# Performance work log

Measured on AMD Instinct MI355X. Metric: run time of the kernel, lower is better.

## Reference

```python
import jax, jax.numpy as jnp
import numpy as np

N, E, D, H, O = 50000, 800000, 128, 256, 64
BN_EPS = 1e-5


def setup_inputs() -> dict:
    key = jax.random.key(0)
    ks = jax.random.split(key, 12)
    x_indices = jnp.arange(N, dtype=jnp.int64) if jax.config.jax_enable_x64 else jnp.arange(N, dtype=jnp.int32)
    ei = jax.random.randint(ks[0], (2, E), 0, N, dtype=jnp.int32)
    s = lambda k, shape, fan: jax.random.normal(k, shape, dtype=jnp.float32) * (1.0 / np.sqrt(fan))
    return {
        "x_indices": x_indices,
        "ei": ei,
        "emb": jax.random.normal(ks[1], (N, D), dtype=jnp.float32),
        "W1": s(ks[2], (D, H), D), "b1": jnp.zeros((H,), jnp.float32),
        "g1": jnp.ones((H,), jnp.float32), "be1": jnp.zeros((H,), jnp.float32),
        "W2": s(ks[3], (H, H), H), "b2": jnp.zeros((H,), jnp.float32),
        "g2": jnp.ones((H,), jnp.float32), "be2": jnp.zeros((H,), jnp.float32),
        "W3": s(ks[4], (H, O), H), "b3": jnp.zeros((O,), jnp.float32),
    }


def reference(x_indices, ei, emb, W1, b1, g1, be1, W2, b2, g2, be2, W3, b3):
    n = emb.shape[0]
    # GCN normalization with self-loops (PyG GCNConv default):
    loop = jnp.arange(n, dtype=ei.dtype)
    row = jnp.concatenate([ei[0], loop])  # source
    col = jnp.concatenate([ei[1], loop])  # target (aggregation index)
    deg = jax.ops.segment_sum(jnp.ones_like(col, dtype=emb.dtype), col, num_segments=n)
    dinv = jnp.where(deg > 0, 1.0 / jnp.sqrt(jnp.maximum(deg, 1.0)), 0.0)
    norm = dinv[row] * dinv[col]  # [E+N]

    def conv(x, W, b):
        xl = x @ W                                   # [N, d_out]
        msg = xl[row] * norm[:, None]                # gather + scale
        return jax.ops.segment_sum(msg, col, num_segments=n) + b  # scatter-add

    def bn(x, g, be):  # batch-stat BatchNorm1d (training-mode stats)
        m = jnp.mean(x, axis=0)
        v = jnp.var(x, axis=0)
        return (x - m) * (g / jnp.sqrt(v + BN_EPS)) + be

    x = emb[x_indices]
    x = jax.nn.relu(bn(conv(x, W1, b1), g1, be1))
    x = jax.nn.relu(bn(conv(x, W2, b2), g2, be2))
    return conv(x, W3, b3)
```

## Files before the change

kernel.cpp:

```cpp
#include <hip/hip_runtime.h>
#include <hip/hip_bf16.h>

#define Dk 128
#define Hk 256
#define Ok 64
#define BN_EPS 1e-5f
#define NSLICE 64

typedef __attribute__((ext_vector_type(8))) short short8;
typedef __attribute__((ext_vector_type(4))) float f32x4;

static __device__ __forceinline__ float bf2f(ushort u) {
    union { uint32_t i; float f; } c; c.i = ((uint32_t)u) << 16; return c.f;
}
static __device__ __forceinline__ ushort f2bf(float f) {
    union { float f; uint32_t u; } c; c.f = f;
    return (ushort)((c.u + 0x7fffu + ((c.u >> 16) & 1u)) >> 16);
}


#define W1SZ (Dk * Hk)
#define W2SZ (Hk * Hk)
#define W3SZ (Hk * Ok)
#define WBLK ((W1SZ + W2SZ + W3SZ) / 256)
#define STATSP_FLOATS (2 * NSLICE * 512)

__global__ void count_cvt_kernel(const int* __restrict__ ecol, int* __restrict__ cnt, int E,
                                 const float* __restrict__ emb, const int* __restrict__ xidx,
                                 ushort* __restrict__ embb,
                                 const float* __restrict__ W1, const float* __restrict__ W2,
                                 const float* __restrict__ W3, ushort* __restrict__ W1t,
                                 ushort* __restrict__ W2t, ushort* __restrict__ W3t,
                                 float* __restrict__ statsP, int n) {
    const int cntBlocks = (E + 255) >> 8;
    const int embBlocks = (n * (Dk / 8) + 255) >> 8;
    int bid = blockIdx.x;
    if (bid < cntBlocks) {
        int e = bid * 256 + threadIdx.x;
        if (e < E) atomicAdd(&cnt[ecol[e]], 1);
        return;
    }
    bid -= cntBlocks;
    if (bid < embBlocks) {
        int gid = bid * 256 + threadIdx.x;
        int total = n * (Dk / 8);
        if (gid >= total) return;
        int node = gid >> 4, seg = gid & 15;
        int src = xidx[node];
        const float* p = &emb[(size_t)src * Dk + seg * 8];
        float4 lo = *(const float4*)p, hi = *(const float4*)(p + 4);
        ushort r[8] = {f2bf(lo.x), f2bf(lo.y), f2bf(lo.z), f2bf(lo.w),
                       f2bf(hi.x), f2bf(hi.y), f2bf(hi.z), f2bf(hi.w)};
        *(short8*)&embb[(size_t)gid * 8] = *(short8*)r;
        return;
    }
    bid -= embBlocks;
    if (bid < WBLK) {
        int gid = bid * 256 + threadIdx.x;
        if (gid < W1SZ) {
            int c = gid / Dk, k = gid - c * Dk;
            W1t[gid] = f2bf(W1[(size_t)k * Hk + c]);
        } else if (gid < W1SZ + W2SZ) {
            int idx = gid - W1SZ;
            int c = idx / Hk, k = idx - c * Hk;
            W2t[idx] = f2bf(W2[(size_t)k * Hk + c]);
        } else {
            int idx = gid - W1SZ - W2SZ;
            int c = idx / Hk, k = idx - c * Hk;
            W3t[idx] = f2bf(W3[(size_t)k * Ok + c]);
        }
        return;
    }
    bid -= WBLK;
    int idx = bid * 1024 + threadIdx.x * 4;
    if (idx < STATSP_FLOATS)
        *(float4*)&statsP[idx] = make_float4(0.f, 0.f, 0.f, 0.f);
}

__global__ void dinv_bsum_kernel(const int* __restrict__ cnt, float* __restrict__ dinv,
                                 int* __restrict__ fillc, int* __restrict__ bsum, int n) {
    __shared__ int sm[256];
    int i = blockIdx.x * 256 + threadIdx.x;
    int c = (i < n) ? cnt[i] : 0;
    if (i < n) { dinv[i] = rsqrtf((float)c + 1.0f); fillc[i] = 0; }
    sm[threadIdx.x] = c;
    __syncthreads();
    for (int s = 128; s; s >>= 1) {
        if (threadIdx.x < s) sm[threadIdx.x] += sm[threadIdx.x + s];
        __syncthreads();
    }
    if (!threadIdx.x) bsum[blockIdx.x] = sm[0];
}

__global__ void scan_off_kernel(const int* __restrict__ cnt, const int* __restrict__ bsum,
                                int* __restrict__ offv, int n) {
    __shared__ int sm[256];
    __shared__ int sbase;
    int t = threadIdx.x, bidx = blockIdx.x;
    int part = 0;
    for (int j = t; j < bidx; j += 256) part += bsum[j];
    sm[t] = part;
    __syncthreads();
    for (int s = 128; s; s >>= 1) {
        if (t < s) sm[t] += sm[t + s];
        __syncthreads();
    }
    if (t == 0) sbase = sm[0];
    __syncthreads();
    int base = sbase;
    __syncthreads();
    int i = bidx * 256 + t;
    int v = (i < n) ? cnt[i] : 0;
    sm[t] = v;
    __syncthreads();
    for (int s = 1; s < 256; s <<= 1) {
        int add = (t >= s) ? sm[t - s] : 0;
        __syncthreads();
        sm[t] += add;
        __syncthreads();
    }
    if (i < n) offv[i + 1] = base + sm[t];
    if (i == 0) offv[0] = 0;
}

__global__ void fill_kernel(const int* __restrict__ row, const int* __restrict__ col,
                            const int* __restrict__ off, int* __restrict__ fillc,
                            const float* __restrict__ dinv, int2* __restrict__ ep, int E) {
    int e = blockIdx.x * blockDim.x + threadIdx.x;
    if (e < E) {
        int c = col[e], r = row[e];
        int p = atomicAdd(&fillc[c], 1);
        ep[off[c] + p] = make_int2(r, __float_as_int(dinv[r]));
    }
}

__global__ void bn_finalize_kernel(const float* __restrict__ statsP, const float* __restrict__ g,
                                   const float* __restrict__ be, float* __restrict__ ss,
                                   float invn) {
    int f = threadIdx.x;
    float sum = 0.f, sq = 0.f;
    for (int s = 0; s < NSLICE; ++s) {
        sum += statsP[s * 512 + f];
        sq  += statsP[s * 512 + 256 + f];
    }
    float mean = sum * invn;
    float var = sq * invn - mean * mean;
    float sc = g[f] * rsqrtf(var + BN_EPS);
    ss[f] = sc;
    ss[256 + f] = fmaf(-mean, sc, be[f]);
}


template<int KD, int BNT, bool STATS, bool BIAS, bool BN_A>
__global__ __launch_bounds__(256) void gemm128(
    const ushort* __restrict__ A, const ushort* __restrict__ Wt,
    ushort* __restrict__ Cout, int n, int Hout,
    const float* __restrict__ bias, float* __restrict__ statsP,
    const float* __restrict__ ss)
{
    constexpr int WN = (BNT == 128) ? 2 : 1;
    constexpr int MR = (BNT == 128) ? 4 : 2;
    constexpr int NR = 4;
    constexpr int TILE = (128 + BNT) * 32;
    constexpr int NT = KD / 32;
    __shared__ ushort lds[2 * TILE];
    __shared__ float ssc[BN_A ? KD : 1];
    __shared__ float ssh[BN_A ? KD : 1];

    const int tid = threadIdx.x;
    const int lane = tid & 63, wid = tid >> 6;
    const int wr = wid / WN, wc = wid % WN;
    const int lr = lane & 15, lg = lane >> 4;
    const int bm = blockIdx.x * 128;
    const int bn = blockIdx.y * BNT;

    if (BN_A) {
        for (int f = tid; f < KD; f += 256) {
            ssc[f] = ss[f];
            ssh[f] = ss[KD + f];
        }
        __syncthreads();
    }

    auto stage = [&](int buf, int k0) {
        ushort* As = lds + buf * TILE;
        ushort* Bs = As + 128 * 32;
        #pragma unroll
        for (int c = 0; c < 2; ++c) {
            int boff = wid * 2048 + c * 1024 + lane * 16;
            int row = boff >> 6;
            int k8 = (boff >> 4) & 3;
            int grow = bm + row; if (grow >= n) grow = n - 1;
            const ushort* src = &A[(size_t)grow * KD + k0 + k8 * 8];
            if (BN_A) {
                short8 av = *(const short8*)src;
                ushort r[8];
                #pragma unroll
                for (int j = 0; j < 8; ++j) {
                    int kf = k0 + k8 * 8 + j;
                    float v = bf2f((ushort)av[j]);
                    r[j] = f2bf(fmaxf(fmaf(v, ssc[kf], ssh[kf]), 0.f));
                }
                *(short8*)&As[row * 32 + k8 * 8] = *(short8*)r;
            } else {
                __builtin_amdgcn_global_load_lds(
                    (const __attribute__((address_space(1))) void*)src,
                    (__attribute__((address_space(3))) void*)&As[(wid * 2048 + c * 1024) >> 1],
                    16, 0, 0);
            }
        }
        constexpr int BC = BNT * 64 / 4096;
        #pragma unroll
        for (int c = 0; c < BC; ++c) {
            int boff = wid * (BNT * 16) + c * 1024 + lane * 16;
            int col = boff >> 6;
            int k8 = (boff >> 4) & 3;
            const ushort* src = &Wt[(size_t)(bn + col) * KD + k0 + k8 * 8];
            __builtin_amdgcn_global_load_lds(
                (const __attribute__((address_space(1))) void*)src,
                (__attribute__((address_space(3))) void*)&Bs[(wid * (BNT * 16) + c * 1024) >> 1],
                16, 0, 0);
        }
    };

    f32x4 acc[MR][NR] = {};

    stage(0, 0);
    __syncthreads();
    int cur = 0;
    for (int t = 0; t < NT; ++t) {
        if (t + 1 < NT) stage(cur ^ 1, (t + 1) * 32);
        ushort* As = lds + cur * TILE;
        ushort* Bs = As + 128 * 32;
        short8 af[MR], bfr[NR];
        #pragma unroll
        for (int m = 0; m < MR; ++m)
            af[m] = *(const short8*)&As[(wr * MR * 16 + m * 16 + lr) * 32 + lg * 8];
        #pragma unroll
        for (int nn = 0; nn < NR; ++nn)
            bfr[nn] = *(const short8*)&Bs[(wc * NR * 16 + nn * 16 + lr) * 32 + lg * 8];
        #pragma unroll
        for (int m = 0; m < MR; ++m)
            #pragma unroll
            for (int nn = 0; nn < NR; ++nn)
                acc[m][nn] = __builtin_amdgcn_mfma_f32_16x16x32_bf16(af[m], bfr[nn], acc[m][nn], 0, 0, 0);
        __syncthreads();
        cur ^= 1;
    }

    float s[NR], q[NR];
    #pragma unroll
    for (int nn = 0; nn < NR; ++nn) { s[nn] = 0.f; q[nn] = 0.f; }
    #pragma unroll
    for (int nn = 0; nn < NR; ++nn) {
        int col = bn + wc * NR * 16 + nn * 16 + lr;
        float bv = BIAS ? bias[col] : 0.f;
        #pragma unroll
        for (int m = 0; m < MR; ++m) {
            #pragma unroll
            for (int i = 0; i < 4; ++i) {
                int row = bm + wr * MR * 16 + m * 16 + lg * 4 + i;
                if (row < n) {
                    float v = acc[m][nn][i] + bv;
                    Cout[(size_t)row * Hout + col] = f2bf(v);
                    if (STATS) { s[nn] += v; q[nn] += v * v; }
                }
            }
        }
    }
    if (STATS) {
        float* sp = statsP + (size_t)(blockIdx.x & (NSLICE - 1)) * 512;
        #pragma unroll
        for (int nn = 0; nn < NR; ++nn) {
            s[nn] += __shfl_xor(s[nn], 16);
            q[nn] += __shfl_xor(q[nn], 16);
            s[nn] += __shfl_xor(s[nn], 32);
            q[nn] += __shfl_xor(q[nn], 32);
            if (lg == 0) {
                int col = bn + wc * NR * 16 + nn * 16 + lr;
                atomicAdd(&sp[col], s[nn]);
                atomicAdd(&sp[256 + col], q[nn]);
            }
        }
    }
}


template<int FH, int EPI, int MODE>
__global__ __launch_bounds__(256) void agg_kernel(
    const ushort* __restrict__ x, const int2* __restrict__ ep, const int* __restrict__ off,
    const float* __restrict__ dinv, const float* __restrict__ ss,
    const float* __restrict__ bias, void* __restrict__ outp, int n)
{
    constexpr int LPG = 64 / EPI;
    constexpr int VEC = FH / LPG;
    constexpr int U = 8 / EPI;
    const int tid = threadIdx.x;
    const int lane = tid & 63;
    const int wid = __builtin_amdgcn_readfirstlane(tid >> 6);
    const int node = blockIdx.x * 4 + wid;
    if (node >= n) return;
    const int grp = lane / LPG;
    const int flane = lane % LPG;
    const int fb = flane * VEC;
    const ushort* __restrict__ xb = x + fb;

    float sc[VEC], sh[VEC];
    if (MODE == 1) {
        float4 c4 = *(const float4*)&ss[fb];
        float4 h4 = *(const float4*)&ss[FH + fb];
        sc[0] = c4.x; sc[1] = c4.y; sc[2] = c4.z; sc[3] = c4.w;
        sh[0] = h4.x; sh[1] = h4.y; sh[2] = h4.z; sh[3] = h4.w;
    }
    auto xform = [&](ushort u, int v) -> float {
        float val = bf2f(u);
        if (MODE == 1) val = fmaxf(fmaf(val, sc[v], sh[v]), 0.f);
        return val;
    };

    float di = dinv[node];
    float acc[VEC] = {0.f, 0.f, 0.f, 0.f};
    if (EPI == 1 || grp == 0) {
        ushort4 t = *(const ushort4*)&xb[(size_t)node * FH];
        acc[0] = di * xform(t.x, 0); acc[1] = di * xform(t.y, 1);
        acc[2] = di * xform(t.z, 2); acc[3] = di * xform(t.w, 3);
    }
    const int e1 = off[node + 1];
    int b = off[node];
    for (; b + 8 <= e1; b += 8) {
        int2 p[U];
        ushort4 t[U];
        #pragma unroll
        for (int u = 0; u < U; ++u) p[u] = ep[b + grp + u * EPI];
        #pragma unroll
        for (int u = 0; u < U; ++u) t[u] = *(const ushort4*)&xb[(size_t)p[u].x * FH];
        #pragma unroll
        for (int u = 0; u < U; ++u) {
            float w = __int_as_float(p[u].y);
            acc[0] = fmaf(w, xform(t[u].x, 0), acc[0]);
            acc[1] = fmaf(w, xform(t[u].y, 1), acc[1]);
            acc[2] = fmaf(w, xform(t[u].z, 2), acc[2]);
            acc[3] = fmaf(w, xform(t[u].w, 3), acc[3]);
        }
    }
    if (EPI < 4) {
        for (; b + 2 * EPI <= e1; b += 2 * EPI) {
            int2 p0 = ep[b + grp], p1 = ep[b + grp + EPI];
            ushort4 t0 = *(const ushort4*)&xb[(size_t)p0.x * FH];
            ushort4 t1 = *(const ushort4*)&xb[(size_t)p1.x * FH];
            float w0 = __int_as_float(p0.y), w1 = __int_as_float(p1.y);
            acc[0] = fmaf(w0, xform(t0.x, 0), acc[0]); acc[1] = fmaf(w0, xform(t0.y, 1), acc[1]);
            acc[2] = fmaf(w0, xform(t0.z, 2), acc[2]); acc[3] = fmaf(w0, xform(t0.w, 3), acc[3]);
            acc[0] = fmaf(w1, xform(t1.x, 0), acc[0]); acc[1] = fmaf(w1, xform(t1.y, 1), acc[1]);
            acc[2] = fmaf(w1, xform(t1.z, 2), acc[2]); acc[3] = fmaf(w1, xform(t1.w, 3), acc[3]);
        }
    }
    for (; b < e1; b += EPI) {
        int idx = b + grp;
        bool ok = idx < e1;
        int2 pp = ep[ok ? idx : e1 - 1];
        ushort4 tt = *(const ushort4*)&xb[(size_t)pp.x * FH];
        float w = ok ? __int_as_float(pp.y) : 0.f;
        acc[0] = fmaf(w, xform(tt.x, 0), acc[0]); acc[1] = fmaf(w, xform(tt.y, 1), acc[1]);
        acc[2] = fmaf(w, xform(tt.z, 2), acc[2]); acc[3] = fmaf(w, xform(tt.w, 3), acc[3]);
    }
    if (EPI == 4) {
        #pragma unroll
        for (int v = 0; v < VEC; ++v) acc[v] += __shfl_xor(acc[v], 16);
    }
    if (EPI >= 2) {
        #pragma unroll
        for (int v = 0; v < VEC; ++v) acc[v] += __shfl_xor(acc[v], 32);
    }
    if (grp == 0) {
        if (MODE == 2) {
            float4 bv = *(const float4*)&bias[fb];
            float4 res;
            res.x = fmaf(di, acc[0], bv.x); res.y = fmaf(di, acc[1], bv.y);
            res.z = fmaf(di, acc[2], bv.z); res.w = fmaf(di, acc[3], bv.w);
            *(float4*)((float*)outp + (size_t)node * FH + fb) = res;
        } else {
            ushort4 o;
            o.x = f2bf(di * acc[0]); o.y = f2bf(di * acc[1]);
            o.z = f2bf(di * acc[2]); o.w = f2bf(di * acc[3]);
            *(ushort4*)((ushort*)outp + (size_t)node * FH + fb) = o;
        }
    }
}


extern "C" void kernel_launch(void* const* d_in, const int* in_sizes, int n_in,
                              void* d_out, int out_size, void* d_ws, size_t ws_size,
                              hipStream_t stream) {
    const int*   x_idx = (const int*)d_in[0];
    const int*   ei    = (const int*)d_in[1];
    const float* emb   = (const float*)d_in[2];
    const float* W1    = (const float*)d_in[3];
    const float* b1    = (const float*)d_in[4];
    const float* g1    = (const float*)d_in[5];
    const float* be1   = (const float*)d_in[6];
    const float* W2    = (const float*)d_in[7];
    const float* b2    = (const float*)d_in[8];
    const float* g2    = (const float*)d_in[9];
    const float* be2   = (const float*)d_in[10];
    const float* W3    = (const float*)d_in[11];
    const float* b3    = (const float*)d_in[12];

    const int N = in_sizes[0];
    const int E = in_sizes[1] / 2;
    const int* erow = ei;
    const int* ecol = ei + E;

    char* p = (char*)d_ws;
    auto alloc = [&](size_t bytes) { char* q = p; p += (bytes + 255) & ~(size_t)255; return q; };
    const int nb = (N + 255) / 256;
    float*  dinv  = (float*) alloc((size_t)N * 4);
    int*    cnt   = (int*)   alloc((size_t)N * 4);
    int*    off   = (int*)   alloc((size_t)(N + 1) * 4);
    int*    fillc = (int*)   alloc((size_t)N * 4);
    int*    bsum  = (int*)   alloc((size_t)nb * 4);
    int2*   ep    = (int2*)  alloc((size_t)E * 8);
    float*  statsP= (float*) alloc((size_t)STATSP_FLOATS * 4);
    float*  stats1P = statsP, *stats2P = statsP + NSLICE * 512;
    float*  ss1   = (float*) alloc(512 * 4);
    float*  ss2   = (float*) alloc(512 * 4);
    ushort* W1t   = (ushort*)alloc((size_t)Dk * Hk * 2);
    ushort* W2t   = (ushort*)alloc((size_t)Hk * Hk * 2);
    ushort* W3t   = (ushort*)alloc((size_t)Hk * Ok * 2);
    ushort* bufU  = (ushort*)alloc((size_t)N * Hk * 2);
    ushort* embb  = bufU;
    ushort* agg1b = bufU + (size_t)N * Dk;
    ushort* conv2b= bufU;
    ushort* conv1b= (ushort*)alloc((size_t)N * Hk * 2);
    ushort* agg2b = (ushort*)alloc((size_t)N * Hk * 2);
    ushort* xl3b  = (ushort*)alloc((size_t)N * Ok * 2);

    const float invn = 1.0f / (float)N;

    hipMemsetAsync(cnt, 0, (size_t)N * 4, stream);
    const int cntBlocks = (E + 255) / 256;
    const int embBlocks = (N * (Dk / 8) + 255) / 256;
    count_cvt_kernel<<<cntBlocks + embBlocks + WBLK + (STATSP_FLOATS + 1023) / 1024,
                       256, 0, stream>>>(
        ecol, cnt, E, emb, x_idx, embb, W1, W2, W3, W1t, W2t, W3t, statsP, N);
    dinv_bsum_kernel<<<nb, 256, 0, stream>>>(cnt, dinv, fillc, bsum, N);
    scan_off_kernel<<<nb, 256, 0, stream>>>(cnt, bsum, off, N);
    fill_kernel<<<(E + 255) / 256, 256, 0, stream>>>(erow, ecol, off, fillc, dinv, ep, E);

    const int rb128 = (N + 127) / 128;
    const int aggBlocks = (N + 3) / 4;

    agg_kernel<Dk, 2, 0><<<aggBlocks, 256, 0, stream>>>(
        embb, ep, off, dinv, nullptr, nullptr, agg1b, N);
    gemm128<Dk, 128, true, true, false><<<dim3(rb128, Hk / 128), 256, 0, stream>>>(
        agg1b, W1t, conv1b, N, Hk, b1, stats1P, nullptr);
    bn_finalize_kernel<<<1, 256, 0, stream>>>(stats1P, g1, be1, ss1, invn);

    agg_kernel<Hk, 1, 1><<<aggBlocks, 256, 0, stream>>>(
        conv1b, ep, off, dinv, ss1, nullptr, agg2b, N);
    gemm128<Hk, 128, true, true, false><<<dim3(rb128, Hk / 128), 256, 0, stream>>>(
        agg2b, W2t, conv2b, N, Hk, b2, stats2P, nullptr);
    bn_finalize_kernel<<<1, 256, 0, stream>>>(stats2P, g2, be2, ss2, invn);

    gemm128<Hk, 64, false, false, true><<<dim3(rb128, 1), 256, 0, stream>>>(
        conv2b, W3t, xl3b, N, Ok, nullptr, nullptr, ss2);
    agg_kernel<Ok, 4, 2><<<aggBlocks, 256, 0, stream>>>(
        xl3b, ep, off, dinv, nullptr, b3, d_out, N);
}
```

Measured before the change: 293.6 us.

## Store intermediate features in 32-column slices to localize aggregation gathers

Intermediate bf16 feature matrices are now stored as column slices of 32 features (slice-major, then node), written by the embedding conversion and the GEMM epilogue and read by the GEMM A-loader and a new slice-based aggregation kernel. Each aggregation block handles one slice for four nodes, so the randomly gathered neighbor rows touch a much smaller working set per slice and may hit cache more often. In exchange, each gather is a 64-byte row segment with only 4-byte loads per lane, the edge list is re-read once per slice, and the GEMM output stores become strided per slice.

```diff
diff --git a/kernel.cpp b/kernel.cpp
--- a/kernel.cpp
+++ b/kernel.cpp
@@ -51,7 +51,8 @@
         float4 lo = *(const float4*)p, hi = *(const float4*)(p + 4);
         ushort r[8] = {f2bf(lo.x), f2bf(lo.y), f2bf(lo.z), f2bf(lo.w),
                        f2bf(hi.x), f2bf(hi.y), f2bf(hi.z), f2bf(hi.w)};
-        *(short8*)&embb[(size_t)gid * 8] = *(short8*)r;
+        int slice = seg >> 2, k8 = seg & 3;
+        *(short8*)&embb[(size_t)slice * n * 32 + (size_t)node * 32 + k8 * 8] = *(short8*)r;
         return;
     }
     bid -= embBlocks;
@@ -173,6 +174,7 @@
     const int lr = lane & 15, lg = lane >> 4;
     const int bm = blockIdx.x * 128;
     const int bn = blockIdx.y * BNT;
+    const size_t sstr = (size_t)n * 32;
 
     if (BN_A) {
         for (int f = tid; f < KD; f += 256) {
@@ -185,13 +187,14 @@
     auto stage = [&](int buf, int k0) {
         ushort* As = lds + buf * TILE;
         ushort* Bs = As + 128 * 32;
+        const ushort* Aslice = A + (size_t)(k0 >> 5) * sstr;
         #pragma unroll
         for (int c = 0; c < 2; ++c) {
             int boff = wid * 2048 + c * 1024 + lane * 16;
             int row = boff >> 6;
             int k8 = (boff >> 4) & 3;
             int grow = bm + row; if (grow >= n) grow = n - 1;
-            const ushort* src = &A[(size_t)grow * KD + k0 + k8 * 8];
+            const ushort* src = &Aslice[(size_t)grow * 32 + k8 * 8];
             if (BN_A) {
                 short8 av = *(const short8*)src;
                 ushort r[8];
@@ -255,6 +258,7 @@
     for (int nn = 0; nn < NR; ++nn) {
         int col = bn + wc * NR * 16 + nn * 16 + lr;
         float bv = BIAS ? bias[col] : 0.f;
+        ushort* Cslice = Cout + (size_t)(col >> 5) * sstr + (col & 31);
         #pragma unroll
         for (int m = 0; m < MR; ++m) {
             #pragma unroll
@@ -262,7 +266,7 @@
                 int row = bm + wr * MR * 16 + m * 16 + lg * 4 + i;
                 if (row < n) {
                     float v = acc[m][nn][i] + bv;
-                    Cout[(size_t)row * Hout + col] = f2bf(v);
+                    Cslice[(size_t)row * 32] = f2bf(v);
                     if (STATS) { s[nn] += v; q[nn] += v * v; }
                 }
             }
@@ -286,104 +290,71 @@
 }
 
 
-template<int FH, int EPI, int MODE>
-__global__ __launch_bounds__(256) void agg_kernel(
+template<int FH, int MODE>
+__global__ __launch_bounds__(256) void agg_slice(
     const ushort* __restrict__ x, const int2* __restrict__ ep, const int* __restrict__ off,
     const float* __restrict__ dinv, const float* __restrict__ ss,
     const float* __restrict__ bias, void* __restrict__ outp, int n)
 {
-    constexpr int LPG = 64 / EPI;
-    constexpr int VEC = FH / LPG;
-    constexpr int U = 8 / EPI;
-    const int tid = threadIdx.x;
-    const int lane = tid & 63;
-    const int wid = __builtin_amdgcn_readfirstlane(tid >> 6);
-    const int node = blockIdx.x * 4 + wid;
+    constexpr int SLICES = FH / 32;
+    const int bid = blockIdx.x;
+    const int slice = bid % SLICES;
+    const int node = (bid / SLICES) * 4 + (threadIdx.x >> 6);
     if (node >= n) return;
-    const int grp = lane / LPG;
-    const int flane = lane % LPG;
-    const int fb = flane * VEC;
-    const ushort* __restrict__ xb = x + fb;
-
-    float sc[VEC], sh[VEC];
+    const int lane = threadIdx.x & 63;
+    const int grp = lane >> 4;
+    const int f2 = (lane & 15) * 2;
+    const ushort* __restrict__ xs = x + (size_t)slice * n * 32 + f2;
+
+    float sc0 = 0.f, sc1 = 0.f, sh0 = 0.f, sh1 = 0.f;
     if (MODE == 1) {
-        float4 c4 = *(const float4*)&ss[fb];
-        float4 h4 = *(const float4*)&ss[FH + fb];
-        sc[0] = c4.x; sc[1] = c4.y; sc[2] = c4.z; sc[3] = c4.w;
-        sh[0] = h4.x; sh[1] = h4.y; sh[2] = h4.z; sh[3] = h4.w;
-    }
-    auto xform = [&](ushort u, int v) -> float {
+        int f = slice * 32 + f2;
+        float2 c2 = *(const float2*)&ss[f];
+        float2 h2 = *(const float2*)&ss[FH + f];
+        sc0 = c2.x; sc1 = c2.y; sh0 = h2.x; sh1 = h2.y;
+    }
+    auto xf = [&](ushort u, int v) -> float {
         float val = bf2f(u);
-        if (MODE == 1) val = fmaxf(fmaf(val, sc[v], sh[v]), 0.f);
+        if (MODE == 1) val = fmaxf(fmaf(val, v ? sc1 : sc0, v ? sh1 : sh0), 0.f);
         return val;
     };
 
     float di = dinv[node];
-    float acc[VEC] = {0.f, 0.f, 0.f, 0.f};
-    if (EPI == 1 || grp == 0) {
-        ushort4 t = *(const ushort4*)&xb[(size_t)node * FH];
-        acc[0] = di * xform(t.x, 0); acc[1] = di * xform(t.y, 1);
-        acc[2] = di * xform(t.z, 2); acc[3] = di * xform(t.w, 3);
+    float a0 = 0.f, a1 = 0.f;
+    if (grp == 0) {
+        ushort2 t = *(const ushort2*)&xs[(size_t)node * 32];
+        a0 = di * xf(t.x, 0); a1 = di * xf(t.y, 1);
     }
     const int e1 = off[node + 1];
     int b = off[node];
     for (; b + 8 <= e1; b += 8) {
-        int2 p[U];
-        ushort4 t[U];
-        #pragma unroll
-        for (int u = 0; u < U; ++u) p[u] = ep[b + grp + u * EPI];
-        #pragma unroll
-        for (int u = 0; u < U; ++u) t[u] = *(const ushort4*)&xb[(size_t)p[u].x * FH];
-        #pragma unroll
-        for (int u = 0; u < U; ++u) {
-            float w = __int_as_float(p[u].y);
-            acc[0] = fmaf(w, xform(t[u].x, 0), acc[0]);
-            acc[1] = fmaf(w, xform(t[u].y, 1), acc[1]);
-            acc[2] = fmaf(w, xform(t[u].z, 2), acc[2]);
-            acc[3] = fmaf(w, xform(t[u].w, 3), acc[3]);
-        }
-    }
-    if (EPI < 4) {
-        for (; b + 2 * EPI <= e1; b += 2 * EPI) {
-            int2 p0 = ep[b + grp], p1 = ep[b + grp + EPI];
-            ushort4 t0 = *(const ushort4*)&xb[(size_t)p0.x * FH];
-            ushort4 t1 = *(const ushort4*)&xb[(size_t)p1.x * FH];
-            float w0 = __int_as_float(p0.y), w1 = __int_as_float(p1.y);
-            acc[0] = fmaf(w0, xform(t0.x, 0), acc[0]); acc[1] = fmaf(w0, xform(t0.y, 1), acc[1]);
-            acc[2] = fmaf(w0, xform(t0.z, 2), acc[2]); acc[3] = fmaf(w0, xform(t0.w, 3), acc[3]);
-            acc[0] = fmaf(w1, xform(t1.x, 0), acc[0]); acc[1] = fmaf(w1, xform(t1.y, 1), acc[1]);
-            acc[2] = fmaf(w1, xform(t1.z, 2), acc[2]); acc[3] = fmaf(w1, xform(t1.w, 3), acc[3]);
-        }
-    }
-    for (; b < e1; b += EPI) {
+        int2 p0 = ep[b + grp], p1 = ep[b + grp + 4];
+        ushort2 t0 = *(const ushort2*)&xs[(size_t)p0.x * 32];
+        ushort2 t1 = *(const ushort2*)&xs[(size_t)p1.x * 32];
+        float w0 = __int_as_float(p0.y), w1 = __int_as_float(p1.y);
+        a0 = fmaf(w0, xf(t0.x, 0), a0); a1 = fmaf(w0, xf(t0.y, 1), a1);
+        a0 = fmaf(w1, xf(t1.x, 0), a0); a1 = fmaf(w1, xf(t1.y, 1), a1);
+    }
+    for (; b < e1; b += 4) {
         int idx = b + grp;
         bool ok = idx < e1;
         int2 pp = ep[ok ? idx : e1 - 1];
-        ushort4 tt = *(const ushort4*)&xb[(size_t)pp.x * FH];
+        ushort2 tt = *(const ushort2*)&xs[(size_t)pp.x * 32];
         float w = ok ? __int_as_float(pp.y) : 0.f;
-        acc[0] = fmaf(w, xform(tt.x, 0), acc[0]); acc[1] = fmaf(w, xform(tt.y, 1), acc[1]);
-        acc[2] = fmaf(w, xform(tt.z, 2), acc[2]); acc[3] = fmaf(w, xform(tt.w, 3), acc[3]);
-    }
-    if (EPI == 4) {
-        #pragma unroll
-        for (int v = 0; v < VEC; ++v) acc[v] += __shfl_xor(acc[v], 16);
-    }
-    if (EPI >= 2) {
-        #pragma unroll
-        for (int v = 0; v < VEC; ++v) acc[v] += __shfl_xor(acc[v], 32);
-    }
+        a0 = fmaf(w, xf(tt.x, 0), a0); a1 = fmaf(w, xf(tt.y, 1), a1);
+    }
+    a0 += __shfl_xor(a0, 16); a1 += __shfl_xor(a1, 16);
+    a0 += __shfl_xor(a0, 32); a1 += __shfl_xor(a1, 32);
     if (grp == 0) {
         if (MODE == 2) {
-            float4 bv = *(const float4*)&bias[fb];
-            float4 res;
-            res.x = fmaf(di, acc[0], bv.x); res.y = fmaf(di, acc[1], bv.y);
-            res.z = fmaf(di, acc[2], bv.z); res.w = fmaf(di, acc[3], bv.w);
-            *(float4*)((float*)outp + (size_t)node * FH + fb) = res;
+            int f = slice * 32 + f2;
+            float2 bv = *(const float2*)&bias[f];
+            float2 res = make_float2(fmaf(di, a0, bv.x), fmaf(di, a1, bv.y));
+            *(float2*)((float*)outp + (size_t)node * FH + f) = res;
         } else {
-            ushort4 o;
-            o.x = f2bf(di * acc[0]); o.y = f2bf(di * acc[1]);
-            o.z = f2bf(di * acc[2]); o.w = f2bf(di * acc[3]);
-            *(ushort4*)((ushort*)outp + (size_t)node * FH + fb) = o;
+            ushort2 o;
+            o.x = f2bf(di * a0); o.y = f2bf(di * a1);
+            *(ushort2*)((ushort*)outp + (size_t)slice * n * 32 + (size_t)node * 32 + f2) = o;
         }
     }
 }
@@ -448,15 +419,15 @@
     fill_kernel<<<(E + 255) / 256, 256, 0, stream>>>(erow, ecol, off, fillc, dinv, ep, E);
 
     const int rb128 = (N + 127) / 128;
-    const int aggBlocks = (N + 3) / 4;
-
-    agg_kernel<Dk, 2, 0><<<aggBlocks, 256, 0, stream>>>(
+    const int nbNodes = (N + 3) / 4;
+
+    agg_slice<Dk, 0><<<4 * nbNodes, 256, 0, stream>>>(
         embb, ep, off, dinv, nullptr, nullptr, agg1b, N);
     gemm128<Dk, 128, true, true, false><<<dim3(rb128, Hk / 128), 256, 0, stream>>>(
         agg1b, W1t, conv1b, N, Hk, b1, stats1P, nullptr);
     bn_finalize_kernel<<<1, 256, 0, stream>>>(stats1P, g1, be1, ss1, invn);
 
-    agg_kernel<Hk, 1, 1><<<aggBlocks, 256, 0, stream>>>(
+    agg_slice<Hk, 1><<<8 * nbNodes, 256, 0, stream>>>(
         conv1b, ep, off, dinv, ss1, nullptr, agg2b, N);
     gemm128<Hk, 128, true, true, false><<<dim3(rb128, Hk / 128), 256, 0, stream>>>(
         agg2b, W2t, conv2b, N, Hk, b2, stats2P, nullptr);
@@ -464,6 +435,6 @@
 
     gemm128<Hk, 64, false, false, true><<<dim3(rb128, 1), 256, 0, stream>>>(
         conv2b, W3t, xl3b, N, Ok, nullptr, nullptr, ss2);
-    agg_kernel<Ok, 4, 2><<<aggBlocks, 256, 0, stream>>>(
+    agg_slice<Ok, 2><<<2 * nbNodes, 256, 0, stream>>>(
         xl3b, ep, off, dinv, nullptr, b3, d_out, N);
 }
```

Result: slower. 449.2 us (+53.0%).
